# Performance work log

Measured on AMD Instinct MI355X. Metric: run time of the kernel, lower is better.

## Reference

```python
import jax, jax.numpy as jnp
import numpy as np

N_SUPPORT = 4096
N_QUERY = 8192
H = W = 28
IN_DIM = H * W  # 784
EMBED_DIM = 512
N_CLASSES = 64


def setup_inputs() -> dict:
    key = jax.random.key(0)
    k1, k2, k3, k4 = jax.random.split(key, 4)
    support_set = jax.random.normal(k1, (N_SUPPORT, 1, H, W), dtype=jnp.float32)
    query_set = jax.random.normal(k2, (N_QUERY, 1, H, W), dtype=jnp.float32)
    # one-hot support labels (N, C)
    lbl = jax.random.randint(k3, (N_SUPPORT,), 0, N_CLASSES)
    support_labels = jax.nn.one_hot(lbl, N_CLASSES, dtype=jnp.float32)
    # encoder params: flatten + dense projection stand-in for embedding_net
    W_enc = jax.random.normal(k4, (IN_DIM, EMBED_DIM), dtype=jnp.float32) * (1.0 / np.sqrt(IN_DIM))
    b_enc = jnp.zeros((EMBED_DIM,), dtype=jnp.float32)
    return {
        "support_set": support_set,
        "query_set": query_set,
        "support_labels": support_labels,
        "W_enc": W_enc,
        "b_enc": b_enc,
    }


def _encode(x, W_enc, b_enc):
    # (B, 1, H, W) -> (B, D): flatten + linear projection
    B = x.shape[0]
    return x.reshape(B, -1) @ W_enc + b_enc


def _neg_cdist(q, s):
    # -euclidean distance, computed via the expansion ||q-s||^2 = |q|^2 + |s|^2 - 2 q.s
    q2 = jnp.sum(q * q, axis=-1, keepdims=True)          # (Q, 1)
    s2 = jnp.sum(s * s, axis=-1)[None, :]                # (1, N)
    qs = jnp.einsum("qd,nd->qn", q, s)                  # (Q, N)
    d2 = jnp.maximum(q2 + s2 - 2.0 * qs, 0.0)
    return -jnp.sqrt(d2)


def reference(support_set, query_set, support_labels, W_enc, b_enc):
    support_emb = _encode(support_set, W_enc, b_enc)     # (N, D)
    query_emb = _encode(query_set, W_enc, b_enc)         # (Q, D)
    distances = _neg_cdist(query_emb, support_emb)       # (Q, N)
    attention = jax.nn.softmax(distances, axis=1)        # (Q, N)
    predictions = attention @ support_labels             # (Q, C)
    return predictions
```

## Files before the change

### kernel.cpp

```cpp
#include <hip/hip_runtime.h>

#define N_SUP 4096
#define N_QRY 8192
#define IN_DIM 784
#define EMB 512
#define NCLS 64
#define M_TOT (N_SUP + N_QRY)
#define NCHUNK 25
#define XCH 13

typedef _Float16 f16;
typedef _Float16 f16x8 __attribute__((ext_vector_type(8)));
typedef float f32x4 __attribute__((ext_vector_type(4)));

#define GLDS16(gp, lp)                                                        \
    __builtin_amdgcn_global_load_lds(                                         \
        (const __attribute__((address_space(1))) void*)(gp),                  \
        (__attribute__((address_space(3))) void*)(lp), 16, 0, 0)

static __device__ __forceinline__ f16x8 cvt8(const float* p) {
    float4 a = *(const float4*)p;
    float4 b = *(const float4*)(p + 4);
    f16x8 v;
    v[0] = (f16)a.x; v[1] = (f16)a.y; v[2] = (f16)a.z; v[3] = (f16)a.w;
    v[4] = (f16)b.x; v[5] = (f16)b.y; v[6] = (f16)b.z; v[7] = (f16)b.w;
    return v;
}

__global__ __launch_bounds__(256) void prep_wb(const float* __restrict__ W,
                                               f16* __restrict__ Wb) {
    int g = blockIdx.x * 256 + threadIdx.x;
    if (g >= NCHUNK * 32 * 64) return;
    int chunk = g >> 11;
    int rem = g & 2047;
    int nbg = rem >> 6, lane = rem & 63;
    int n = nbg * 16 + (lane & 15);
    int kbase = chunk * 32 + (lane >> 4) * 8;
    f16x8 v;
#pragma unroll
    for (int j = 0; j < 8; ++j) {
        int k = kbase + j;
        v[j] = (k < IN_DIM) ? (f16)W[(size_t)k * EMB + n] : (f16)0.f;
    }
    *(f16x8*)(Wb + (size_t)g * 8) = v;
}

__global__ __launch_bounds__(256) void prep_lbl(const float* __restrict__ lab,
                                                int* __restrict__ lbl) {
    const int w = threadIdx.x >> 6, lane = threadIdx.x & 63;
    const int s = blockIdx.x * 4 + w;
    float v = lab[(size_t)s * NCLS + lane];
    int c = lane;
#pragma unroll
    for (int off = 1; off < 64; off <<= 1) {
        float v2 = __shfl_xor(v, off);
        int c2 = __shfl_xor(c, off);
        if (v2 > v || (v2 == v && c2 < c)) { v = v2; c = c2; }
    }
    if (lane == 0) lbl[s] = c;
}

__global__ __launch_bounds__(256) void prep_L(const int* __restrict__ lbl,
                                              f16* __restrict__ Lcs) {
    int idx = blockIdx.x * 256 + threadIdx.x;
    if (idx >= NCLS * N_SUP) return;
    int c = idx >> 12, s = idx & (N_SUP - 1);
    Lcs[idx] = (lbl[s] == c) ? (f16)1.f : (f16)0.f;
}

__global__ __launch_bounds__(256) void prep_sb(const f16* __restrict__ E,
                                               f16* __restrict__ Sb) {
    int g = blockIdx.x * 256 + threadIdx.x;
    int s = g >> 6, lg = g & 63;
    f16x8 v = *(const f16x8*)(E + (size_t)s * EMB + lg * 8);
    *(f16x8*)(Sb + (size_t)s * EMB + ((lg ^ (s & 15)) * 8)) = v;
}

__global__ __launch_bounds__(256) void encode(
    const float* __restrict__ sup, const float* __restrict__ qry,
    const f16* __restrict__ Wb, const float* __restrict__ bias,
    f16* __restrict__ E, float* __restrict__ norms)
{
    __shared__ __align__(16) f16 Xs[32][72];
    const int tid = threadIdx.x;
    const int w = tid >> 6, lane = tid & 63;
    const int q = lane >> 4, c16 = lane & 15;
    const int mb = blockIdx.x >> 1;
    const int ch = blockIdx.x & 1;
    const int m0 = mb * 32;
    const int rbase = (w & 1) * 16;
    const int nbg0 = ch * 16 + (w >> 1) * 8;
    const int cbase = nbg0 * 16;

    f32x4 acc[8];
#pragma unroll
    for (int nb = 0; nb < 8; ++nb) acc[nb] = (f32x4){0.f, 0.f, 0.f, 0.f};

    const int sr = tid >> 3;
    const int sq = tid & 7;
    const float* xrow;
    {
        int gr = m0 + sr;
        xrow = (gr < N_SUP) ? sup + (size_t)gr * IN_DIM
                            : qry + (size_t)(gr - N_SUP) * IN_DIM;
    }

    f16x8 xg = cvt8(xrow + sq * 8);

    for (int c = 0; c < XCH; ++c) {
        __syncthreads();
        *(f16x8*)&Xs[sr][sq * 8] = xg;
        __syncthreads();
        if (c + 1 < XCH) {
            int k = (c + 1) * 64 + sq * 8;
            xg = (k + 8 <= IN_DIM) ? cvt8(xrow + k) : (f16x8){0,0,0,0,0,0,0,0};
        }
#pragma unroll
        for (int kc = 0; kc < 2; ++kc) {
            int c32 = c * 2 + kc;
            if (c32 >= NCHUNK) break;
            f16x8 a = *(const f16x8*)&Xs[rbase + c16][kc * 32 + q * 8];
            const f16* wb = Wb + ((size_t)(c32 * 32 + nbg0) * 64 + lane) * 8;
#pragma unroll
            for (int nb = 0; nb < 8; ++nb) {
                f16x8 b = *(const f16x8*)(wb + (size_t)nb * 512);
                acc[nb] = __builtin_amdgcn_mfma_f32_16x16x32_f16(a, b, acc[nb], 0, 0, 0);
            }
        }
    }

    float nrm[4] = {0.f, 0.f, 0.f, 0.f};
#pragma unroll
    for (int nb = 0; nb < 8; ++nb) {
        int col = cbase + nb * 16 + c16;
        float bv = bias[col];
#pragma unroll
        for (int r = 0; r < 4; ++r) {
            int row = m0 + rbase + q * 4 + r;
            float v = acc[nb][r] + bv;
            E[(size_t)row * EMB + col] = (f16)v;
            nrm[r] += v * v;
        }
    }
#pragma unroll
    for (int r = 0; r < 4; ++r) {
        float v = nrm[r];
        v += __shfl_xor(v, 1); v += __shfl_xor(v, 2);
        v += __shfl_xor(v, 4); v += __shfl_xor(v, 8);
        if (c16 == 0) atomicAdd(&norms[m0 + rbase + q * 4 + r], v);
    }
}

__global__ __launch_bounds__(256) void anchor(const f16* __restrict__ E,
                                              const float* __restrict__ norms,
                                              float* __restrict__ manc) {
    const int w = threadIdx.x >> 6, lane = threadIdx.x & 63;
    const int qrow = blockIdx.x * 4 + w;
    f16x8 qv = *(const f16x8*)(E + (size_t)(N_SUP + qrow) * EMB + lane * 8);
    f16x8 sv = *(const f16x8*)(E + lane * 8);
    float dot = 0.f;
#pragma unroll
    for (int j = 0; j < 8; ++j) dot += (float)qv[j] * (float)sv[j];
    dot += __shfl_xor(dot, 1);  dot += __shfl_xor(dot, 2);
    dot += __shfl_xor(dot, 4);  dot += __shfl_xor(dot, 8);
    dot += __shfl_xor(dot, 16); dot += __shfl_xor(dot, 32);
    if (lane == 0) {
        float d2 = fmaxf(norms[N_SUP + qrow] + norms[0] - 2.f * dot, 0.f);
        manc[qrow] = sqrtf(d2);
    }
}

__global__ __launch_bounds__(256, 3) void attn(
    const f16* __restrict__ E, const float* __restrict__ norms,
    const float* __restrict__ manc, const f16* __restrict__ Lcs,
    const f16* __restrict__ Sb, float* __restrict__ Num)
{
    __shared__ __align__(16) f16 Ss[2][16 * EMB];
    __shared__ __align__(16) f16 Pt[4][16][40];
    __shared__ float Sn[512];
    const int tid = threadIdx.x;
    const int w = tid >> 6, lane = tid & 63;
    const int q = lane >> 4, c16 = lane & 15;
    const int ss = blockIdx.x & 7;
    const int qt = blockIdx.x >> 3;

    Sn[tid]       = norms[ss * 512 + tid];
    Sn[256 + tid] = norms[ss * 512 + 256 + tid];

    f16x8 qf[16];
    const f16* qb = E + (size_t)(N_SUP + qt * 64 + w * 16 + c16) * EMB + q * 8;
#pragma unroll
    for (int ks = 0; ks < 16; ++ks) qf[ks] = *(const f16x8*)(qb + ks * 32);
    float q2[4], mrow[4];
#pragma unroll
    for (int r = 0; r < 4; ++r) {
        q2[r]   = norms[N_SUP + qt * 64 + w * 16 + q * 4 + r];
        mrow[r] = manc[qt * 64 + w * 16 + q * 4 + r];
    }

    f32x4 accPL[4];
#pragma unroll
    for (int nb = 0; nb < 4; ++nb) accPL[nb] = (f32x4){0.f, 0.f, 0.f, 0.f};

    const f16* sb_base = Sb + (size_t)(ss * 512) * EMB;
    const int wslot = w * 256;

#pragma unroll
    for (int i = 0; i < 4; ++i)
        GLDS16(sb_base + (size_t)(wslot + i * 64 + lane) * 8,
               &Ss[0][(wslot + i * 64) * 8]);
    __syncthreads();

#pragma unroll 2
    for (int t = 0; t < 32; ++t) {
        const int cur = t & 1;
        if (t + 1 < 32) {
            const f16* gsrc = sb_base + (size_t)(t + 1) * 16 * EMB;
#pragma unroll
            for (int i = 0; i < 4; ++i)
                GLDS16(gsrc + (size_t)(wslot + i * 64 + lane) * 8,
                       &Ss[cur ^ 1][(wslot + i * 64) * 8]);
        }
        f16x8 bl[4];
        if (t & 1) {
            const int ps0 = ss * 512 + (t >> 1) * 32;
#pragma unroll
            for (int nbc = 0; nbc < 4; ++nbc)
                bl[nbc] = *(const f16x8*)(Lcs + (size_t)(nbc * 16 + c16) * N_SUP + ps0 + q * 8);
        }

        f32x4 accQK = (f32x4){0.f, 0.f, 0.f, 0.f};
#pragma unroll
        for (int kc = 0; kc < 4; ++kc) {
#pragma unroll
            for (int ksl = 0; ksl < 4; ++ksl) {
                const int lg = kc * 16 + ksl * 4 + q;
                f16x8 b = *(const f16x8*)&Ss[cur][c16 * EMB + ((lg ^ c16) * 8)];
                accQK = __builtin_amdgcn_mfma_f32_16x16x32_f16(
                    qf[kc * 4 + ksl], b, accQK, 0, 0, 0);
            }
        }
        {
            const float s2 = Sn[t * 16 + c16];
            const int pcol = (t & 1) * 16 + c16;
#pragma unroll
            for (int r = 0; r < 4; ++r) {
                float d2 = fmaxf(q2[r] + s2 - 2.f * accQK[r], 0.f);
                float p = __expf(mrow[r] - __builtin_amdgcn_sqrtf(d2));
                p = fminf(p, 60000.f);
                Pt[w][q * 4 + r][pcol] = (f16)p;
            }
        }
        if (t & 1) {
            f16x8 af = *(const f16x8*)&Pt[w][c16][q * 8];
#pragma unroll
            for (int nbc = 0; nbc < 4; ++nbc)
                accPL[nbc] = __builtin_amdgcn_mfma_f32_16x16x32_f16(af, bl[nbc], accPL[nbc], 0, 0, 0);
        }

        __syncthreads();
    }

#pragma unroll
    for (int nbc = 0; nbc < 4; ++nbc)
#pragma unroll
        for (int r = 0; r < 4; ++r)
            atomicAdd(&Num[(size_t)(qt * 64 + w * 16 + q * 4 + r) * NCLS + nbc * 16 + c16],
                      accPL[nbc][r]);
}

__global__ __launch_bounds__(256) void finalize(const float* __restrict__ Num,
                                                float* __restrict__ out) {
    const int tid = threadIdx.x;
    const int w = tid >> 6, lane = tid & 63;
    const int qrow = blockIdx.x * 4 + w;
    float v = Num[(size_t)qrow * NCLS + lane];
    float s = v;
    s += __shfl_xor(s, 1);  s += __shfl_xor(s, 2);  s += __shfl_xor(s, 4);
    s += __shfl_xor(s, 8);  s += __shfl_xor(s, 16); s += __shfl_xor(s, 32);
    out[(size_t)qrow * NCLS + lane] = v / s;
}

extern "C" void kernel_launch(void* const* d_in, const int* in_sizes, int n_in,
                              void* d_out, int out_size, void* d_ws, size_t ws_size,
                              hipStream_t stream) {
    (void)in_sizes; (void)n_in; (void)out_size; (void)ws_size;
    const float* sup  = (const float*)d_in[0];
    const float* qry  = (const float*)d_in[1];
    const float* lab  = (const float*)d_in[2];
    const float* Wenc = (const float*)d_in[3];
    const float* benc = (const float*)d_in[4];
    float* out = (float*)d_out;

    char* ws = (char*)d_ws;
    size_t off = 0;
    f16* Wb = (f16*)(ws + off);        off += (size_t)NCHUNK * 32 * 64 * 8 * 2;
    f16* E  = (f16*)(ws + off);        off += (size_t)M_TOT * EMB * 2;
    f16* Sb = (f16*)(ws + off);        off += (size_t)N_SUP * EMB * 2;
    int* lbl = (int*)(ws + off);       off += (size_t)N_SUP * 4;
    f16* Lcs = (f16*)(ws + off);       off += (size_t)NCLS * N_SUP * 2;
    float* manc = (float*)(ws + off);  off += (size_t)N_QRY * 4;
    float* norms = (float*)(ws + off); off += (size_t)M_TOT * 4;
    float* Num = (float*)(ws + off);   off += (size_t)N_QRY * NCLS * 4;

    hipMemsetAsync(norms, 0, (size_t)M_TOT * 4 + (size_t)N_QRY * NCLS * 4, stream);

    prep_wb<<<(NCHUNK * 32 * 64 + 255) / 256, 256, 0, stream>>>(Wenc, Wb);
    prep_lbl<<<N_SUP / 4, 256, 0, stream>>>(lab, lbl);
    prep_L<<<NCLS * N_SUP / 256, 256, 0, stream>>>(lbl, Lcs);
    encode<<<M_TOT / 32 * 2, 256, 0, stream>>>(sup, qry, Wb, benc, E, norms);
    prep_sb<<<N_SUP * 64 / 256, 256, 0, stream>>>(E, Sb);
    anchor<<<N_QRY / 4, 256, 0, stream>>>(E, norms, manc);
    attn<<<N_QRY / 64 * 8, 256, 0, stream>>>(E, norms, manc, Lcs, Sb, Num);
    finalize<<<N_QRY / 4, 256, 0, stream>>>(Num, out);
}
```

Measured before the change: 199.3 us.

## Merge small prep kernels and software-pipeline QK MFMA with softmax epilogue

The small preprocessing kernels are merged into two launches (pre_enc, post_enc), one on each side of encode, which removes several kernel launch gaps. The attention main loop is restructured to process tile pairs. The QK MFMA for the next tile is issued at raised wave priority while the exp/sqrt epilogue and the PV MFMA of the previous tile run, so matrix and vector work can overlap. Label loads in the PV step are now issued right before their MFMAs instead of being prefetched, which may add load latency. The extra live accumulators may also raise register pressure against the occupancy target of 3.

```diff
diff --git a/kernel.cpp b/kernel.cpp
--- a/kernel.cpp
+++ b/kernel.cpp
@@ -27,53 +27,38 @@
     return v;
 }
 
-__global__ __launch_bounds__(256) void prep_wb(const float* __restrict__ W,
-                                               f16* __restrict__ Wb) {
-    int g = blockIdx.x * 256 + threadIdx.x;
-    if (g >= NCHUNK * 32 * 64) return;
-    int chunk = g >> 11;
-    int rem = g & 2047;
-    int nbg = rem >> 6, lane = rem & 63;
-    int n = nbg * 16 + (lane & 15);
-    int kbase = chunk * 32 + (lane >> 4) * 8;
-    f16x8 v;
-#pragma unroll
-    for (int j = 0; j < 8; ++j) {
-        int k = kbase + j;
-        v[j] = (k < IN_DIM) ? (f16)W[(size_t)k * EMB + n] : (f16)0.f;
-    }
-    *(f16x8*)(Wb + (size_t)g * 8) = v;
-}
-
-__global__ __launch_bounds__(256) void prep_lbl(const float* __restrict__ lab,
-                                                int* __restrict__ lbl) {
-    const int w = threadIdx.x >> 6, lane = threadIdx.x & 63;
-    const int s = blockIdx.x * 4 + w;
-    float v = lab[(size_t)s * NCLS + lane];
-    int c = lane;
-#pragma unroll
-    for (int off = 1; off < 64; off <<= 1) {
-        float v2 = __shfl_xor(v, off);
-        int c2 = __shfl_xor(c, off);
-        if (v2 > v || (v2 == v && c2 < c)) { v = v2; c = c2; }
-    }
-    if (lane == 0) lbl[s] = c;
-}
-
-__global__ __launch_bounds__(256) void prep_L(const int* __restrict__ lbl,
-                                              f16* __restrict__ Lcs) {
-    int idx = blockIdx.x * 256 + threadIdx.x;
-    if (idx >= NCLS * N_SUP) return;
-    int c = idx >> 12, s = idx & (N_SUP - 1);
-    Lcs[idx] = (lbl[s] == c) ? (f16)1.f : (f16)0.f;
-}
-
-__global__ __launch_bounds__(256) void prep_sb(const f16* __restrict__ E,
-                                               f16* __restrict__ Sb) {
-    int g = blockIdx.x * 256 + threadIdx.x;
-    int s = g >> 6, lg = g & 63;
-    f16x8 v = *(const f16x8*)(E + (size_t)s * EMB + lg * 8);
-    *(f16x8*)(Sb + (size_t)s * EMB + ((lg ^ (s & 15)) * 8)) = v;
+__global__ __launch_bounds__(256) void pre_enc(const float* __restrict__ W,
+                                               const float* __restrict__ lab,
+                                               f16* __restrict__ Wb,
+                                               int* __restrict__ lbl) {
+    if (blockIdx.x < 200) {
+        int g = blockIdx.x * 256 + threadIdx.x;
+        if (g >= NCHUNK * 32 * 64) return;
+        int chunk = g >> 11;
+        int rem = g & 2047;
+        int nbg = rem >> 6, lane = rem & 63;
+        int n = nbg * 16 + (lane & 15);
+        int kbase = chunk * 32 + (lane >> 4) * 8;
+        f16x8 v;
+#pragma unroll
+        for (int j = 0; j < 8; ++j) {
+            int k = kbase + j;
+            v[j] = (k < IN_DIM) ? (f16)W[(size_t)k * EMB + n] : (f16)0.f;
+        }
+        *(f16x8*)(Wb + (size_t)g * 8) = v;
+    } else {
+        const int w = threadIdx.x >> 6, lane = threadIdx.x & 63;
+        const int s = (blockIdx.x - 200) * 4 + w;
+        float v = lab[(size_t)s * NCLS + lane];
+        int c = lane;
+#pragma unroll
+        for (int off = 1; off < 64; off <<= 1) {
+            float v2 = __shfl_xor(v, off);
+            int c2 = __shfl_xor(c, off);
+            if (v2 > v || (v2 == v && c2 < c)) { v = v2; c = c2; }
+        }
+        if (lane == 0) lbl[s] = c;
+    }
 }
 
 __global__ __launch_bounds__(256) void encode(
@@ -151,22 +136,75 @@
     }
 }
 
-__global__ __launch_bounds__(256) void anchor(const f16* __restrict__ E,
-                                              const float* __restrict__ norms,
-                                              float* __restrict__ manc) {
-    const int w = threadIdx.x >> 6, lane = threadIdx.x & 63;
-    const int qrow = blockIdx.x * 4 + w;
-    f16x8 qv = *(const f16x8*)(E + (size_t)(N_SUP + qrow) * EMB + lane * 8);
-    f16x8 sv = *(const f16x8*)(E + lane * 8);
-    float dot = 0.f;
-#pragma unroll
-    for (int j = 0; j < 8; ++j) dot += (float)qv[j] * (float)sv[j];
-    dot += __shfl_xor(dot, 1);  dot += __shfl_xor(dot, 2);
-    dot += __shfl_xor(dot, 4);  dot += __shfl_xor(dot, 8);
-    dot += __shfl_xor(dot, 16); dot += __shfl_xor(dot, 32);
-    if (lane == 0) {
-        float d2 = fmaxf(norms[N_SUP + qrow] + norms[0] - 2.f * dot, 0.f);
-        manc[qrow] = sqrtf(d2);
+__global__ __launch_bounds__(256) void post_enc(
+    const f16* __restrict__ E, const float* __restrict__ norms,
+    const int* __restrict__ lbl, f16* __restrict__ Sb,
+    f16* __restrict__ Lcs, float* __restrict__ manc)
+{
+    const int b = blockIdx.x;
+    if (b < 1024) {
+        int g = b * 256 + threadIdx.x;
+        int s = g >> 6, lg = g & 63;
+        f16x8 v = *(const f16x8*)(E + (size_t)s * EMB + lg * 8);
+        *(f16x8*)(Sb + (size_t)s * EMB + ((lg ^ (s & 15)) * 8)) = v;
+    } else if (b < 3072) {
+        const int w = threadIdx.x >> 6, lane = threadIdx.x & 63;
+        const int qrow = (b - 1024) * 4 + w;
+        f16x8 qv = *(const f16x8*)(E + (size_t)(N_SUP + qrow) * EMB + lane * 8);
+        f16x8 sv = *(const f16x8*)(E + lane * 8);
+        float dot = 0.f;
+#pragma unroll
+        for (int j = 0; j < 8; ++j) dot += (float)qv[j] * (float)sv[j];
+        dot += __shfl_xor(dot, 1);  dot += __shfl_xor(dot, 2);
+        dot += __shfl_xor(dot, 4);  dot += __shfl_xor(dot, 8);
+        dot += __shfl_xor(dot, 16); dot += __shfl_xor(dot, 32);
+        if (lane == 0) {
+            float d2 = fmaxf(norms[N_SUP + qrow] + norms[0] - 2.f * dot, 0.f);
+            manc[qrow] = sqrtf(d2);
+        }
+    } else {
+        int idx = (b - 3072) * 256 + threadIdx.x;
+        int c = idx >> 12, s = idx & (N_SUP - 1);
+        Lcs[idx] = (lbl[s] == c) ? (f16)1.f : (f16)0.f;
+    }
+}
+
+static __device__ __forceinline__ f32x4 qk16(const f16* S, const f16x8* qf,
+                                             int q, int c16) {
+    f32x4 a = (f32x4){0.f, 0.f, 0.f, 0.f};
+#pragma unroll
+    for (int kc = 0; kc < 4; ++kc)
+#pragma unroll
+        for (int ksl = 0; ksl < 4; ++ksl) {
+            const int lg = kc * 16 + ksl * 4 + q;
+            f16x8 b = *(const f16x8*)&S[c16 * EMB + ((lg ^ c16) * 8)];
+            a = __builtin_amdgcn_mfma_f32_16x16x32_f16(qf[kc * 4 + ksl], b, a, 0, 0, 0);
+        }
+    return a;
+}
+
+static __device__ __forceinline__ void epi(f32x4 acc, int t, f32x4 q2, f32x4 mrow,
+                                           const float* Sn, f16 (*PtW)[40],
+                                           int q, int c16) {
+    const float s2 = Sn[t * 16 + c16];
+    const int pcol = (t & 1) * 16 + c16;
+#pragma unroll
+    for (int r = 0; r < 4; ++r) {
+        float d2 = fmaxf(q2[r] + s2 - 2.f * acc[r], 0.f);
+        float p = __expf(mrow[r] - __builtin_amdgcn_sqrtf(d2));
+        PtW[q * 4 + r][pcol] = (f16)fminf(p, 60000.f);
+    }
+}
+
+static __device__ __forceinline__ void pv(f32x4* accPL, const f16* __restrict__ Lcs,
+                                          const f16 (*PtW)[40], int q, int c16,
+                                          int pair, int ss) {
+    const int ps0 = ss * 512 + pair * 32;
+    f16x8 af = *(const f16x8*)&PtW[c16][q * 8];
+#pragma unroll
+    for (int nbc = 0; nbc < 4; ++nbc) {
+        f16x8 bl = *(const f16x8*)(Lcs + (size_t)(nbc * 16 + c16) * N_SUP + ps0 + q * 8);
+        accPL[nbc] = __builtin_amdgcn_mfma_f32_16x16x32_f16(af, bl, accPL[nbc], 0, 0, 0);
     }
 }
 
@@ -191,7 +229,7 @@
     const f16* qb = E + (size_t)(N_SUP + qt * 64 + w * 16 + c16) * EMB + q * 8;
 #pragma unroll
     for (int ks = 0; ks < 16; ++ks) qf[ks] = *(const f16x8*)(qb + ks * 32);
-    float q2[4], mrow[4];
+    f32x4 q2, mrow;
 #pragma unroll
     for (int r = 0; r < 4; ++r) {
         q2[r]   = norms[N_SUP + qt * 64 + w * 16 + q * 4 + r];
@@ -205,61 +243,45 @@
     const f16* sb_base = Sb + (size_t)(ss * 512) * EMB;
     const int wslot = w * 256;
 
-#pragma unroll
-    for (int i = 0; i < 4; ++i)
-        GLDS16(sb_base + (size_t)(wslot + i * 64 + lane) * 8,
-               &Ss[0][(wslot + i * 64) * 8]);
+    const f16* gl = sb_base + (size_t)(wslot + lane) * 8;
+    f16* l0 = &Ss[0][wslot * 8];
+    f16* l1 = &Ss[1][wslot * 8];
+
+#pragma unroll
+    for (int i = 0; i < 4; ++i) GLDS16(gl + i * 512, l0 + i * 512);
     __syncthreads();
-
-#pragma unroll 2
-    for (int t = 0; t < 32; ++t) {
-        const int cur = t & 1;
-        if (t + 1 < 32) {
-            const f16* gsrc = sb_base + (size_t)(t + 1) * 16 * EMB;
-#pragma unroll
-            for (int i = 0; i < 4; ++i)
-                GLDS16(gsrc + (size_t)(wslot + i * 64 + lane) * 8,
-                       &Ss[cur ^ 1][(wslot + i * 64) * 8]);
-        }
-        f16x8 bl[4];
-        if (t & 1) {
-            const int ps0 = ss * 512 + (t >> 1) * 32;
-#pragma unroll
-            for (int nbc = 0; nbc < 4; ++nbc)
-                bl[nbc] = *(const f16x8*)(Lcs + (size_t)(nbc * 16 + c16) * N_SUP + ps0 + q * 8);
-        }
-
-        f32x4 accQK = (f32x4){0.f, 0.f, 0.f, 0.f};
-#pragma unroll
-        for (int kc = 0; kc < 4; ++kc) {
-#pragma unroll
-            for (int ksl = 0; ksl < 4; ++ksl) {
-                const int lg = kc * 16 + ksl * 4 + q;
-                f16x8 b = *(const f16x8*)&Ss[cur][c16 * EMB + ((lg ^ c16) * 8)];
-                accQK = __builtin_amdgcn_mfma_f32_16x16x32_f16(
-                    qf[kc * 4 + ksl], b, accQK, 0, 0, 0);
-            }
-        }
-        {
-            const float s2 = Sn[t * 16 + c16];
-            const int pcol = (t & 1) * 16 + c16;
-#pragma unroll
-            for (int r = 0; r < 4; ++r) {
-                float d2 = fmaxf(q2[r] + s2 - 2.f * accQK[r], 0.f);
-                float p = __expf(mrow[r] - __builtin_amdgcn_sqrtf(d2));
-                p = fminf(p, 60000.f);
-                Pt[w][q * 4 + r][pcol] = (f16)p;
-            }
-        }
-        if (t & 1) {
-            f16x8 af = *(const f16x8*)&Pt[w][c16][q * 8];
-#pragma unroll
-            for (int nbc = 0; nbc < 4; ++nbc)
-                accPL[nbc] = __builtin_amdgcn_mfma_f32_16x16x32_f16(af, bl[nbc], accPL[nbc], 0, 0, 0);
-        }
-
+    gl += 16 * EMB;
+
+    f32x4 accA = (f32x4){0.f, 0.f, 0.f, 0.f};
+    f32x4 accB = (f32x4){0.f, 0.f, 0.f, 0.f};
+
+    for (int tp = 0; tp < 16; ++tp) {
+        const int t0 = tp * 2;
+#pragma unroll
+        for (int i = 0; i < 4; ++i) GLDS16(gl + i * 512, l1 + i * 512);
+        __builtin_amdgcn_s_setprio(1);
+        accA = qk16(&Ss[0][0], qf, q, c16);
+        __builtin_amdgcn_s_setprio(0);
+        if (tp > 0) {
+            epi(accB, t0 - 1, q2, mrow, Sn, Pt[w], q, c16);
+            pv(accPL, Lcs, Pt[w], q, c16, tp - 1, ss);
+        }
         __syncthreads();
-    }
+
+        if (tp < 15) {
+#pragma unroll
+            for (int i = 0; i < 4; ++i) GLDS16(gl + 16 * EMB + i * 512, l0 + i * 512);
+        }
+        __builtin_amdgcn_s_setprio(1);
+        accB = qk16(&Ss[1][0], qf, q, c16);
+        __builtin_amdgcn_s_setprio(0);
+        epi(accA, t0, q2, mrow, Sn, Pt[w], q, c16);
+        __syncthreads();
+
+        gl += 32 * EMB;
+    }
+    epi(accB, 31, q2, mrow, Sn, Pt[w], q, c16);
+    pv(accPL, Lcs, Pt[w], q, c16, 15, ss);
 
 #pragma unroll
     for (int nbc = 0; nbc < 4; ++nbc)
@@ -305,12 +327,9 @@
 
     hipMemsetAsync(norms, 0, (size_t)M_TOT * 4 + (size_t)N_QRY * NCLS * 4, stream);
 
-    prep_wb<<<(NCHUNK * 32 * 64 + 255) / 256, 256, 0, stream>>>(Wenc, Wb);
-    prep_lbl<<<N_SUP / 4, 256, 0, stream>>>(lab, lbl);
-    prep_L<<<NCLS * N_SUP / 256, 256, 0, stream>>>(lbl, Lcs);
+    pre_enc<<<1224, 256, 0, stream>>>(Wenc, lab, Wb, lbl);
     encode<<<M_TOT / 32 * 2, 256, 0, stream>>>(sup, qry, Wb, benc, E, norms);
-    prep_sb<<<N_SUP * 64 / 256, 256, 0, stream>>>(E, Sb);
-    anchor<<<N_QRY / 4, 256, 0, stream>>>(E, norms, manc);
+    post_enc<<<4096, 256, 0, stream>>>(E, norms, lbl, Sb, Lcs, manc);
     attn<<<N_QRY / 64 * 8, 256, 0, stream>>>(E, norms, manc, Lcs, Sb, Num);
     finalize<<<N_QRY / 4, 256, 0, stream>>>(Num, out);
 }
```

Measured after the change: 200.3 us. Within noise of the previous version (+0.5%).
